# Performance work log

Hardware: AMD Instinct MI355X
Metric: run time of the kernel (lower is better)

The kernel has to match this reference:

```python
import jax, jax.numpy as jnp
import numpy as np

T, B, D, H, L = 512, 128, 256, 256, 4
EPS = 1e-5

def _ln(x, g, b):
    m = jnp.mean(x, axis=-1, keepdims=True)
    v = jnp.mean((x - m) ** 2, axis=-1, keepdims=True)
    return (x - m) * jax.lax.rsqrt(v + EPS) * g + b

def setup_inputs() -> dict:
    key = jax.random.key(0)
    ks = jax.random.split(key, 24)
    s = 0.02
    inp = {
        "x": jax.random.normal(ks[0], (T, B, D), dtype=jnp.float32),
        "lengths": jax.random.randint(ks[1], (B,), 1, T + 1, dtype=jnp.int32),
        # LinearEnchancedGRU params
        "Wr": jax.random.normal(ks[2], (D + H, H)) * s,
        "gr": jnp.ones((H,)), "br": jnp.zeros((H,)),
        "Wz": jax.random.normal(ks[3], (D + H, H)) * s,
        "gz": jnp.ones((H,)), "bz": jnp.zeros((H,)),
        "Wl": jax.random.normal(ks[4], (D + H, H)) * s,
        "gl": jnp.ones((H,)), "bl": jnp.zeros((H,)),
        "Wlt": jax.random.normal(ks[5], (D, H)) * s,
        "Cx": jax.random.normal(ks[6], (D, H)) * s,
        "Ch_w": jax.random.normal(ks[7], (H, H)) * s,
        "Ch_b": jnp.zeros((H,)),
        # TransitionGRU stack params [L, ...]
        "tWr": jax.random.normal(ks[8], (L, H, H)) * s,
        "tgr": jnp.ones((L, H)), "tbr": jnp.zeros((L, H)),
        "tWz": jax.random.normal(ks[9], (L, H, H)) * s,
        "tgz": jnp.ones((L, H)), "tbz": jnp.zeros((L, H)),
        "tWc": jax.random.normal(ks[10], (L, H, H)) * s,
        "tbc": jnp.zeros((L, H)),
    }
    return inp

def reference(x, lengths, Wr, gr, br, Wz, gz, bz, Wl, gl, bl, Wlt, Cx, Ch_w, Ch_b,
              tWr, tgr, tbr, tWz, tgz, tbz, tWc, tbc):
    # x: [T,B,D]; lengths: [B]. Packed-sequence semantics: hidden state of a
    # finished example is frozen; its outputs are zero padding.
    mask = jnp.arange(T, dtype=jnp.int32)[:, None] < lengths[None, :]  # [T,B]

    def cell(xt, h):
        cat = jnp.concatenate([xt, h], axis=-1)  # [B, D+H]
        r = jax.nn.sigmoid(_ln(cat @ Wr, gr, br))
        z = jax.nn.sigmoid(_ln(cat @ Wz, gz, bz))
        l = jax.nn.sigmoid(_ln(cat @ Wl, gl, bl))
        n = jnp.tanh(xt @ Cx + r * (h @ Ch_w + Ch_b)) + l * (xt @ Wlt)
        h = (1.0 - z) * h + z * n
        for i in range(L):  # deep transition stack (fixed small depth)
            ri = jax.nn.sigmoid(_ln(h @ tWr[i], tgr[i], tbr[i]))
            zi = jax.nn.sigmoid(_ln(h @ tWz[i], tgz[i], tbz[i]))
            ni = jnp.tanh(ri * (h @ tWc[i] + tbc[i]))
            h = (1.0 - zi) * ni + zi * h
        return h

    def step(h, inputs):
        xt, mt = inputs  # [B,D], [B]
        hn = cell(xt, h)
        hn = jnp.where(mt[:, None], hn, h)
        out = jnp.where(mt[:, None], hn, 0.0)
        return hn, out

    h0 = jnp.zeros((B, H), dtype=x.dtype)
    _, outs = jax.lax.scan(step, h0, (x, mask))  # outs: [T,B,H]
    return outs
```

## Files before the change

### kernel.cpp

```cpp
#include <hip/hip_runtime.h>
#include <hip/hip_bf16.h>

#define T_ 512
#define B_ 128
#define D_ 256
#define H_ 256
#define EPS 1e-5f

typedef __attribute__((ext_vector_type(8))) short short8;
typedef __attribute__((ext_vector_type(4))) short short4v;
typedef __attribute__((ext_vector_type(4))) float f32x4;

#define SLICE_E  86016
#define WT_TOTAL 1376256

#define STATS_OFFB 2752512UL
#define HX_OFFB    2850816UL
#define FLAG_OFFB  2981888UL
#define NFLAGS     512

#define L_XBF  0
#define L_HBF  8192
#define L_G6   16384
#define L_SRED 22528
#define L_AUX  23040
#define L_TRN  47616
#define L_END  145920

__device__ __forceinline__ short f2bf(float f) {
  unsigned u = __builtin_bit_cast(unsigned, f);
  u = (u + 0x7FFFu + ((u >> 16) & 1u)) >> 16;
  return (short)u;
}
__device__ __forceinline__ f32x4 zero4() { f32x4 z = {0.f, 0.f, 0.f, 0.f}; return z; }
__device__ __forceinline__ f32x4 mfma16(short8 a, short8 b, f32x4 c) {
  return __builtin_amdgcn_mfma_f32_16x16x32_bf16(a, b, c, 0, 0, 0);
}
__device__ __forceinline__ void waitv0() { asm volatile("s_waitcnt vmcnt(0)" ::: "memory"); }

__device__ __forceinline__ f32x4 ald4(float* p) {
  unsigned long long* q = (unsigned long long*)p;
  unsigned long long a = __hip_atomic_load(q,     __ATOMIC_RELAXED, __HIP_MEMORY_SCOPE_AGENT);
  unsigned long long b = __hip_atomic_load(q + 1, __ATOMIC_RELAXED, __HIP_MEMORY_SCOPE_AGENT);
  f32x4 v;
  v[0] = __builtin_bit_cast(float, (unsigned)(a & 0xffffffffu));
  v[1] = __builtin_bit_cast(float, (unsigned)(a >> 32));
  v[2] = __builtin_bit_cast(float, (unsigned)(b & 0xffffffffu));
  v[3] = __builtin_bit_cast(float, (unsigned)(b >> 32));
  return v;
}
__device__ __forceinline__ void ast1f(float* p, float v) {
  __hip_atomic_store((unsigned*)p, __builtin_bit_cast(unsigned, v),
                     __ATOMIC_RELAXED, __HIP_MEMORY_SCOPE_AGENT);
}

__global__ void prep_weights(const float* __restrict__ Wr, const float* __restrict__ Wz,
                             const float* __restrict__ Wl, const float* __restrict__ Wlt,
                             const float* __restrict__ Cx, const float* __restrict__ Chw,
                             const float* __restrict__ tWr, const float* __restrict__ tWz,
                             const float* __restrict__ tWc, short* __restrict__ wt) {
  int idx = blockIdx.x * 256 + threadIdx.x;
  if (idx >= WT_TOTAL) return;
  int j  = idx / SLICE_E;
  int r  = idx - j * SLICE_E;
  int u  = r >> 12;
  int rr = r & 4095;
  int kf = rr >> 9;
  int le = rr & 511;
  int l  = le >> 3, e = le & 7;
  int la = l & 15, lh = l >> 4;
  int col = j * 16 + la;
  float v;
  if (u < 6) {
    int g = u >> 1, half = u & 1;
    int k = half * 256 + lh * 8 + kf * 32 + e;
    const float* W = (g == 0) ? Wr : (g == 1 ? Wz : Wl);
    v = W[k * 256 + col];
  } else if (u < 9) {
    int a = u - 6;
    int k = lh * 8 + kf * 32 + e;
    const float* W = (a == 0) ? Cx : (a == 1 ? Wlt : Chw);
    v = W[k * 256 + col];
  } else {
    int q = u - 9;
    int li = q / 3, m = q - li * 3;
    int k = lh * 8 + kf * 32 + e;
    const float* W = (m == 0) ? tWr : (m == 1 ? tWz : tWc);
    v = W[(li * 256 + k) * 256 + col];
  }
  wt[idx] = f2bf(v);
}

__global__ __launch_bounds__(64)
void rnn_sx(const float* __restrict__ x, const int* __restrict__ lengths,
            const float* __restrict__ gr, const float* __restrict__ br,
            const float* __restrict__ gz, const float* __restrict__ bz,
            const float* __restrict__ gl, const float* __restrict__ bl,
            const float* __restrict__ Chb,
            const float* __restrict__ tgr, const float* __restrict__ tbr,
            const float* __restrict__ tgz, const float* __restrict__ tbz,
            const float* __restrict__ tbc,
            const short* __restrict__ W, float* __restrict__ stats,
            short* __restrict__ hxs, unsigned* __restrict__ flags,
            float* __restrict__ out) {

  __shared__ __align__(16) char smem[L_END];

  const int l  = threadIdx.x;
  const int la = l & 15, lh = l >> 4;
  const int amask = (la & 7) << 4;
  const int bid = blockIdx.x;
  const int cl = bid & 7, j = bid >> 3;
  const int rb0 = cl * 16;
  const int myrow = l >> 2, mc = (l & 3) * 4;
  const int cg = j * 16 + mc;
  const int colb = (l & 3) * 64;

  const short* Wsl = W + (size_t)j * SLICE_E;

  #pragma unroll 1
  for (int u = 0; u < 15; ++u) {
    char* dst = smem + ((u < 3) ? (L_AUX + u * 8192) : (L_TRN + (u - 3) * 8192));
    const short* src = Wsl + (size_t)(u + 6) * 4096;
    #pragma unroll
    for (int kf = 0; kf < 8; ++kf)
      *(short8*)(dst + kf * 1024 + l * 16) = *(const short8*)(src + kf * 512 + l * 8);
  }
  for (int i = l; i < 1024; i += 64) ((short4v*)(smem + L_HBF))[i] = (short4v){0, 0, 0, 0};

  int maxlen = 0;
  for (int i = 0; i < 16; ++i) {
    int v = lengths[rb0 + i];
    maxlen = maxlen > v ? maxlen : v;
  }
  const int mylen = lengths[rb0 + myrow];

  float* stc = stats + (size_t)(cl * 2) * 1536;
  short* hxc = hxs + (size_t)(cl * 2) * 4096;
  unsigned* flc = flags + cl * 64;

  f32x4 hreg = zero4();
  int dead = 0;

  auto pollf = [&](unsigned* fb, unsigned tag) {
    if (!dead) {
      int it = 0;
      while (true) {
        unsigned v = tag;
        if (l < 16) v = __hip_atomic_load(fb + l, __ATOMIC_RELAXED, __HIP_MEMORY_SCOPE_AGENT);
        if (__all((int)(v >= tag))) break;
        if (++it > 300000) { dead = 1; break; }
        __builtin_amdgcn_s_sleep(1);
      }
    }
    asm volatile("" ::: "memory");
  };
  auto ldu = [&](short8 (&dst)[8], const short* bp) {
    #pragma unroll
    for (int kf = 0; kf < 8; ++kf) dst[kf] = *(const short8*)(bp + kf * 512 + l * 8);
  };
  auto mm8r = [&](short8 (&Bv)[8], f32x4& acc, int Ab) {
    #pragma unroll
    for (int kf = 0; kf < 8; ++kf) {
      int aoff = Ab + la * 512 + (((kf * 64) + lh * 16) ^ amask);
      acc = mfma16(*(const short8*)(smem + aoff), Bv[kf], acc);
    }
  };
  auto mmlds = [&](int Bub, f32x4& acc, int Ab) {
    #pragma unroll
    for (int kf = 0; kf < 8; ++kf) {
      int aoff = Ab + la * 512 + (((kf * 64) + lh * 16) ^ amask);
      short8 bv = *(const short8*)(smem + Bub + kf * 1024 + l * 16);
      acc = mfma16(*(const short8*)(smem + aoff), bv, acc);
    }
  };
  auto g6store = [&](int arr, f32x4 acc) {
    #pragma unroll
    for (int i = 0; i < 4; ++i)
      *(float*)(smem + L_G6 + ((arr * 16 + lh * 4 + i) * 16 + la) * 4) = acc[i];
  };
  auto readhx = [&](int par) {
    float* hp = (float*)(hxc + par * 4096 + (l >> 2) * 256 + colb);
    int row2 = l >> 2;
    #pragma unroll
    for (int q2 = 0; q2 < 8; ++q2) {
      f32x4 v = ald4(hp + q2 * 4);
      *(f32x4*)(smem + L_HBF + row2 * 512 + ((colb * 2 + q2 * 16) ^ ((row2 & 7) << 4))) = v;
    }
  };
  auto posth = [&](int par) {
    unsigned long long pk =
        (unsigned long long)(unsigned short)f2bf(hreg[0]) |
        ((unsigned long long)(unsigned short)f2bf(hreg[1]) << 16) |
        ((unsigned long long)(unsigned short)f2bf(hreg[2]) << 32) |
        ((unsigned long long)(unsigned short)f2bf(hreg[3]) << 48);
    __hip_atomic_store((unsigned long long*)(hxc + par * 4096 + myrow * 256 + cg), pk,
                       __ATOMIC_RELAXED, __HIP_MEMORY_SCOPE_AGENT);
  };

  short8 B0[8], B1[8];
  ldu(B0, Wsl);
  ldu(B1, Wsl + 4096);

  for (int t = 0; t < maxlen; ++t) {
    int R = t * 5, par = R & 1;
    {
      const float* xs = x + ((size_t)t * B_ + rb0 + (l >> 2)) * D_ + colb;
      int row2 = l >> 2;
      #pragma unroll
      for (int u2 = 0; u2 < 8; ++u2) {
        f32x4 a = *(const f32x4*)(xs + u2 * 8);
        f32x4 b = *(const f32x4*)(xs + u2 * 8 + 4);
        short8 s;
        s[0] = f2bf(a[0]); s[1] = f2bf(a[1]); s[2] = f2bf(a[2]); s[3] = f2bf(a[3]);
        s[4] = f2bf(b[0]); s[5] = f2bf(b[1]); s[6] = f2bf(b[2]); s[7] = f2bf(b[3]);
        *(short8*)(smem + L_XBF + row2 * 512 + ((colb * 2 + u2 * 16) ^ ((row2 & 7) << 4))) = s;
      }
    }
    f32x4 ac[6];
    #pragma unroll
    for (int a2 = 0; a2 < 6; ++a2) ac[a2] = zero4();
    mm8r(B0, ac[0], L_XBF); ldu(B0, Wsl + 2 * 4096);
    mm8r(B1, ac[0], L_HBF); ldu(B1, Wsl + 3 * 4096);
    mm8r(B0, ac[1], L_XBF); ldu(B0, Wsl + 4 * 4096);
    mm8r(B1, ac[1], L_HBF); ldu(B1, Wsl + 5 * 4096);
    mm8r(B0, ac[2], L_XBF);
    mm8r(B1, ac[2], L_HBF);
    mmlds(L_AUX,         ac[3], L_XBF);
    mmlds(L_AUX + 8192,  ac[4], L_XBF);
    mmlds(L_AUX + 16384, ac[5], L_HBF);
    #pragma unroll
    for (int a2 = 0; a2 < 6; ++a2) g6store(a2, ac[a2]);
    f32x4 pv[6];
    #pragma unroll
    for (int a2 = 0; a2 < 6; ++a2)
      pv[a2] = *(const f32x4*)(smem + L_G6 + ((a2 * 16 + myrow) * 16 + mc) * 4);
    float st[6];
    #pragma unroll
    for (int g2 = 0; g2 < 3; ++g2) {
      f32x4 v = pv[g2];
      st[2 * g2]     = v[0] + v[1] + v[2] + v[3];
      st[2 * g2 + 1] = v[0] * v[0] + v[1] * v[1] + v[2] * v[2] + v[3] * v[3];
    }
    #pragma unroll
    for (int s2 = 0; s2 < 6; ++s2) {
      st[s2] += __shfl_xor(st[s2], 1);
      st[s2] += __shfl_xor(st[s2], 2);
    }
    float* sp = stc + par * 1536;
    {
      int k4 = l & 3;
      ast1f(sp + (k4 * 16 + myrow) * 16 + j, st[k4]);
      if (k4 < 2) ast1f(sp + ((4 + k4) * 16 + myrow) * 16 + j, st[4 + k4]);
    }
    waitv0();
    if (l == 0)
      __hip_atomic_store(flc + par * 16 + j, (unsigned)(R + 1),
                         __ATOMIC_RELAXED, __HIP_MEMORY_SCOPE_AGENT);
    pollf(flc + par * 16, (unsigned)(R + 1));
    {
      float* q = sp + l * 16;
      f32x4 a = ald4(q), b = ald4(q + 4), c = ald4(q + 8), d = ald4(q + 12);
      f32x4 s4 = a + b + c + d;
      *(float*)(smem + L_SRED + l * 4) = s4[0] + s4[1] + s4[2] + s4[3];
      if (l < 32) {
        float* q2 = sp + (64 + l) * 16;
        f32x4 a2 = ald4(q2), b2 = ald4(q2 + 4), c2 = ald4(q2 + 8), d2 = ald4(q2 + 12);
        f32x4 t4 = a2 + b2 + c2 + d2;
        *(float*)(smem + L_SRED + (64 + l) * 4) = t4[0] + t4[1] + t4[2] + t4[3];
      }
    }
    {
      float m3[3], rs3[3];
      #pragma unroll
      for (int g2 = 0; g2 < 3; ++g2) {
        float s1 = *(float*)(smem + L_SRED + ((2 * g2) * 16 + myrow) * 4);
        float s2 = *(float*)(smem + L_SRED + ((2 * g2 + 1) * 16 + myrow) * 4);
        float mm = s1 * (1.f / 256.f);
        float vv = s2 * (1.f / 256.f) - mm * mm;
        m3[g2] = mm; rs3[g2] = rsqrtf((vv > 0.f ? vv : 0.f) + EPS);
      }
      f32x4 g4r = *(const f32x4*)(gr + cg), b4r = *(const f32x4*)(br + cg);
      f32x4 g4z = *(const f32x4*)(gz + cg), b4z = *(const f32x4*)(bz + cg);
      f32x4 g4l = *(const f32x4*)(gl + cg), b4l = *(const f32x4*)(bl + cg);
      f32x4 cb4 = *(const f32x4*)(Chb + cg);
      bool act = t < mylen;
      f32x4 hn;
      #pragma unroll
      for (int q2 = 0; q2 < 4; ++q2) {
        float rv = 1.f / (1.f + __expf(-((pv[0][q2] - m3[0]) * rs3[0] * g4r[q2] + b4r[q2])));
        float zv = 1.f / (1.f + __expf(-((pv[1][q2] - m3[1]) * rs3[1] * g4z[q2] + b4z[q2])));
        float lv = 1.f / (1.f + __expf(-((pv[2][q2] - m3[2]) * rs3[2] * g4l[q2] + b4l[q2])));
        float n = tanhf(pv[3][q2] + rv * (pv[5][q2] + cb4[q2])) + lv * pv[4][q2];
        hn[q2] = (1.f - zv) * hreg[q2] + zv * n;
      }
      if (act) hreg = hn;
    }
    posth(par);
    waitv0();
    if (l == 0)
      __hip_atomic_store(flc + (2 + par) * 16 + j, (unsigned)(R + 1),
                         __ATOMIC_RELAXED, __HIP_MEMORY_SCOPE_AGENT);
    pollf(flc + (2 + par) * 16, (unsigned)(R + 1));
    readhx(par);

    #pragma unroll 1
    for (int li = 0; li < 4; ++li) {
      R = t * 5 + 1 + li; par = R & 1;
      f32x4 tc0 = zero4(), tc1 = zero4(), tc2 = zero4();
      mmlds(L_TRN + (li * 3 + 0) * 8192, tc0, L_HBF);
      mmlds(L_TRN + (li * 3 + 1) * 8192, tc1, L_HBF);
      mmlds(L_TRN + (li * 3 + 2) * 8192, tc2, L_HBF);
      g6store(0, tc0); g6store(1, tc1); g6store(2, tc2);
      f32x4 qv[3];
      #pragma unroll
      for (int a2 = 0; a2 < 3; ++a2)
        qv[a2] = *(const f32x4*)(smem + L_G6 + ((a2 * 16 + myrow) * 16 + mc) * 4);
      float st4[4];
      #pragma unroll
      for (int g2 = 0; g2 < 2; ++g2) {
        f32x4 v = qv[g2];
        st4[2 * g2]     = v[0] + v[1] + v[2] + v[3];
        st4[2 * g2 + 1] = v[0] * v[0] + v[1] * v[1] + v[2] * v[2] + v[3] * v[3];
      }
      #pragma unroll
      for (int s2 = 0; s2 < 4; ++s2) {
        st4[s2] += __shfl_xor(st4[s2], 1);
        st4[s2] += __shfl_xor(st4[s2], 2);
      }
      float* sp2 = stc + par * 1536;
      ast1f(sp2 + ((l & 3) * 16 + myrow) * 16 + j, st4[l & 3]);
      waitv0();
      if (l == 0)
        __hip_atomic_store(flc + par * 16 + j, (unsigned)(R + 1),
                           __ATOMIC_RELAXED, __HIP_MEMORY_SCOPE_AGENT);
      if (li == 3) {
        ldu(B0, Wsl);
        ldu(B1, Wsl + 4096);
      }
      pollf(flc + par * 16, (unsigned)(R + 1));
      {
        float* q = sp2 + l * 16;
        f32x4 a = ald4(q), b = ald4(q + 4), c = ald4(q + 8), d = ald4(q + 12);
        f32x4 s4 = a + b + c + d;
        *(float*)(smem + L_SRED + l * 4) = s4[0] + s4[1] + s4[2] + s4[3];
      }
      bool act = t < mylen;
      {
        float m2[2], rs2[2];
        #pragma unroll
        for (int g2 = 0; g2 < 2; ++g2) {
          float s1 = *(float*)(smem + L_SRED + ((2 * g2) * 16 + myrow) * 4);
          float s2 = *(float*)(smem + L_SRED + ((2 * g2 + 1) * 16 + myrow) * 4);
          float mm = s1 * (1.f / 256.f);
          float vv = s2 * (1.f / 256.f) - mm * mm;
          m2[g2] = mm; rs2[g2] = rsqrtf((vv > 0.f ? vv : 0.f) + EPS);
        }
        f32x4 g4r = *(const f32x4*)(tgr + li * 256 + cg), b4r = *(const f32x4*)(tbr + li * 256 + cg);
        f32x4 g4z = *(const f32x4*)(tgz + li * 256 + cg), b4z = *(const f32x4*)(tbz + li * 256 + cg);
        f32x4 cb4 = *(const f32x4*)(tbc + li * 256 + cg);
        f32x4 hn;
        #pragma unroll
        for (int q2 = 0; q2 < 4; ++q2) {
          float rv = 1.f / (1.f + __expf(-((qv[0][q2] - m2[0]) * rs2[0] * g4r[q2] + b4r[q2])));
          float zv = 1.f / (1.f + __expf(-((qv[1][q2] - m2[1]) * rs2[1] * g4z[q2] + b4z[q2])));
          float n = tanhf(rv * (qv[2][q2] + cb4[q2]));
          hn[q2] = (1.f - zv) * n + zv * hreg[q2];
        }
        if (act) hreg = hn;
        if (li == 3) {
          f32x4 o = act ? hreg : zero4();
          *(f32x4*)(out + ((size_t)t * B_ + rb0 + myrow) * H_ + cg) = o;
        }
      }
      posth(par);
      waitv0();
      if (l == 0)
        __hip_atomic_store(flc + (2 + par) * 16 + j, (unsigned)(R + 1),
                           __ATOMIC_RELAXED, __HIP_MEMORY_SCOPE_AGENT);
      pollf(flc + (2 + par) * 16, (unsigned)(R + 1));
      readhx(par);
    }
  }

  for (int t2 = maxlen; t2 < T_; ++t2)
    *(f32x4*)(out + ((size_t)t2 * B_ + rb0 + myrow) * H_ + cg) = zero4();
}

extern "C" void kernel_launch(void* const* d_in, const int* in_sizes, int n_in,
                              void* d_out, int out_size, void* d_ws, size_t ws_size,
                              hipStream_t stream) {
  const float* x    = (const float*)d_in[0];
  const int* lengths = (const int*)d_in[1];
  const float* Wr   = (const float*)d_in[2];
  const float* gr   = (const float*)d_in[3];
  const float* br   = (const float*)d_in[4];
  const float* Wz   = (const float*)d_in[5];
  const float* gz   = (const float*)d_in[6];
  const float* bz   = (const float*)d_in[7];
  const float* Wl   = (const float*)d_in[8];
  const float* gl   = (const float*)d_in[9];
  const float* bl   = (const float*)d_in[10];
  const float* Wlt  = (const float*)d_in[11];
  const float* Cx   = (const float*)d_in[12];
  const float* Chw  = (const float*)d_in[13];
  const float* Chb  = (const float*)d_in[14];
  const float* tWr  = (const float*)d_in[15];
  const float* tgr  = (const float*)d_in[16];
  const float* tbr  = (const float*)d_in[17];
  const float* tWz  = (const float*)d_in[18];
  const float* tgz  = (const float*)d_in[19];
  const float* tbz  = (const float*)d_in[20];
  const float* tWc  = (const float*)d_in[21];
  const float* tbc  = (const float*)d_in[22];

  short*    wt    = (short*)d_ws;
  float*    stats = (float*)((char*)d_ws + STATS_OFFB);
  short*    hxs   = (short*)((char*)d_ws + HX_OFFB);
  unsigned* flags = (unsigned*)((char*)d_ws + FLAG_OFFB);

  hipMemsetAsync(flags, 0, NFLAGS * sizeof(unsigned), stream);
  hipLaunchKernelGGL(prep_weights, dim3((WT_TOTAL + 255) / 256), dim3(256), 0, stream,
                     Wr, Wz, Wl, Wlt, Cx, Chw, tWr, tWz, tWc, wt);
  hipLaunchKernelGGL(rnn_sx, dim3(128), dim3(64), 0, stream,
                     x, lengths, gr, br, gz, bz, gl, bl, Chb,
                     tgr, tbr, tgz, tbz, tbc, wt, stats, hxs, flags, (float*)d_out);
}
```

Before: 17.77 ms.

## Replace flag-based barriers with tagged data words polled directly

Each 32-bit value exchanged between blocks (LayerNorm partial stats and bf16 hidden-state pairs) is packed into a 64-bit word together with a step tag. Consumers poll the data itself until every tag has reached the current step, so the separate flag store, the vmcnt(0) wait and the flag poll before each read are gone. This takes one global round trip off each of the roughly ten cross-block syncs per timestep. In exchange the exchanged data doubles in size, every poll iteration re-reads and reduces the full data set, and the workspace memset grows.

```diff
diff --git a/kernel.cpp b/kernel.cpp
--- a/kernel.cpp
+++ b/kernel.cpp
@@ -10,14 +10,15 @@
 typedef __attribute__((ext_vector_type(8))) short short8;
 typedef __attribute__((ext_vector_type(4))) short short4v;
 typedef __attribute__((ext_vector_type(4))) float f32x4;
+typedef __attribute__((ext_vector_type(4))) unsigned u32x4;
+typedef unsigned long long ull;
 
 #define SLICE_E  86016
 #define WT_TOTAL 1376256
 
 #define STATS_OFFB 2752512UL
-#define HX_OFFB    2850816UL
-#define FLAG_OFFB  2981888UL
-#define NFLAGS     512
+#define HX_OFFB    2949120UL
+#define SYNC_BYTES 458752UL
 
 #define L_XBF  0
 #define L_HBF  8192
@@ -36,22 +37,14 @@
 __device__ __forceinline__ f32x4 mfma16(short8 a, short8 b, f32x4 c) {
   return __builtin_amdgcn_mfma_f32_16x16x32_bf16(a, b, c, 0, 0, 0);
 }
-__device__ __forceinline__ void waitv0() { asm volatile("s_waitcnt vmcnt(0)" ::: "memory"); }
-
-__device__ __forceinline__ f32x4 ald4(float* p) {
-  unsigned long long* q = (unsigned long long*)p;
-  unsigned long long a = __hip_atomic_load(q,     __ATOMIC_RELAXED, __HIP_MEMORY_SCOPE_AGENT);
-  unsigned long long b = __hip_atomic_load(q + 1, __ATOMIC_RELAXED, __HIP_MEMORY_SCOPE_AGENT);
-  f32x4 v;
-  v[0] = __builtin_bit_cast(float, (unsigned)(a & 0xffffffffu));
-  v[1] = __builtin_bit_cast(float, (unsigned)(a >> 32));
-  v[2] = __builtin_bit_cast(float, (unsigned)(b & 0xffffffffu));
-  v[3] = __builtin_bit_cast(float, (unsigned)(b >> 32));
-  return v;
-}
-__device__ __forceinline__ void ast1f(float* p, float v) {
-  __hip_atomic_store((unsigned*)p, __builtin_bit_cast(unsigned, v),
-                     __ATOMIC_RELAXED, __HIP_MEMORY_SCOPE_AGENT);
+__device__ __forceinline__ ull ald8(ull* p) {
+  return __hip_atomic_load(p, __ATOMIC_RELAXED, __HIP_MEMORY_SCOPE_AGENT);
+}
+__device__ __forceinline__ void ast8(ull* p, ull v) {
+  __hip_atomic_store(p, v, __ATOMIC_RELAXED, __HIP_MEMORY_SCOPE_AGENT);
+}
+__device__ __forceinline__ ull pkf(float v, unsigned tag) {
+  return (ull)__builtin_bit_cast(unsigned, v) | ((ull)tag << 32);
 }
 
 __global__ void prep_weights(const float* __restrict__ Wr, const float* __restrict__ Wz,
@@ -100,9 +93,8 @@
             const float* __restrict__ tgr, const float* __restrict__ tbr,
             const float* __restrict__ tgz, const float* __restrict__ tbz,
             const float* __restrict__ tbc,
-            const short* __restrict__ W, float* __restrict__ stats,
-            short* __restrict__ hxs, unsigned* __restrict__ flags,
-            float* __restrict__ out) {
+            const short* __restrict__ W, ull* __restrict__ st8,
+            ull* __restrict__ hx8, float* __restrict__ out) {
 
   __shared__ __align__(16) char smem[L_END];
 
@@ -135,25 +127,78 @@
   }
   const int mylen = lengths[rb0 + myrow];
 
-  float* stc = stats + (size_t)(cl * 2) * 1536;
-  short* hxc = hxs + (size_t)(cl * 2) * 4096;
-  unsigned* flc = flags + cl * 64;
+  ull* stc = st8 + (size_t)cl * 3072;
+  ull* hxc = hx8 + (size_t)cl * 4096;
 
   f32x4 hreg = zero4();
   int dead = 0;
 
-  auto pollf = [&](unsigned* fb, unsigned tag) {
-    if (!dead) {
-      int it = 0;
-      while (true) {
-        unsigned v = tag;
-        if (l < 16) v = __hip_atomic_load(fb + l, __ATOMIC_RELAXED, __HIP_MEMORY_SCOPE_AGENT);
-        if (__all((int)(v >= tag))) break;
-        if (++it > 300000) { dead = 1; break; }
-        __builtin_amdgcn_s_sleep(1);
-      }
-    }
-    asm volatile("" ::: "memory");
+  auto pollred = [&](int par, unsigned tag, bool g6) {
+    ull* p0 = stc + par * 1536 + l * 16;
+    ull* p1 = stc + par * 1536 + (64 + (l & 31)) * 16;
+    float r0 = 0.f, r1 = 0.f;
+    int it = 0;
+    for (;;) {
+      unsigned mn = 0xffffffffu;
+      float a4[4] = {0.f, 0.f, 0.f, 0.f};
+      #pragma unroll
+      for (int k = 0; k < 16; ++k) {
+        ull v = ald8(p0 + k);
+        a4[k & 3] += __builtin_bit_cast(float, (unsigned)v);
+        unsigned tg = (unsigned)(v >> 32);
+        mn = mn < tg ? mn : tg;
+      }
+      r0 = ((a4[0] + a4[1]) + a4[2]) + a4[3];
+      if (g6 && l < 32) {
+        float b4[4] = {0.f, 0.f, 0.f, 0.f};
+        #pragma unroll
+        for (int k = 0; k < 16; ++k) {
+          ull v = ald8(p1 + k);
+          b4[k & 3] += __builtin_bit_cast(float, (unsigned)v);
+          unsigned tg = (unsigned)(v >> 32);
+          mn = mn < tg ? mn : tg;
+        }
+        r1 = ((b4[0] + b4[1]) + b4[2]) + b4[3];
+      }
+      if (__all((int)(mn >= tag)) || dead) break;
+      if (++it > 200000) dead = 1;
+      __builtin_amdgcn_s_sleep(1);
+    }
+    *(float*)(smem + L_SRED + l * 4) = r0;
+    if (g6 && l < 32) *(float*)(smem + L_SRED + 256 + l * 4) = r1;
+  };
+  auto posth = [&](int par, unsigned tag) {
+    unsigned lo0 = (unsigned)(unsigned short)f2bf(hreg[0]) |
+                   ((unsigned)(unsigned short)f2bf(hreg[1]) << 16);
+    unsigned lo1 = (unsigned)(unsigned short)f2bf(hreg[2]) |
+                   ((unsigned)(unsigned short)f2bf(hreg[3]) << 16);
+    ull* hp = hxc + par * 2048 + myrow * 128 + j * 8 + (l & 3) * 2;
+    ast8(hp,     (ull)lo0 | ((ull)tag << 32));
+    ast8(hp + 1, (ull)lo1 | ((ull)tag << 32));
+  };
+  auto readhx = [&](int par, unsigned tag) {
+    int row2 = l >> 2;
+    ull* hp = hxc + par * 2048 + row2 * 128 + (l & 3) * 32;
+    unsigned lo[32];
+    int it = 0;
+    for (;;) {
+      unsigned mn = 0xffffffffu;
+      #pragma unroll
+      for (int k = 0; k < 32; ++k) {
+        ull v = ald8(hp + k);
+        lo[k] = (unsigned)v;
+        unsigned tg = (unsigned)(v >> 32);
+        mn = mn < tg ? mn : tg;
+      }
+      if (__all((int)(mn >= tag)) || dead) break;
+      if (++it > 200000) dead = 1;
+      __builtin_amdgcn_s_sleep(1);
+    }
+    #pragma unroll
+    for (int q = 0; q < 8; ++q) {
+      u32x4 v = { lo[4 * q], lo[4 * q + 1], lo[4 * q + 2], lo[4 * q + 3] };
+      *(u32x4*)(smem + L_HBF + row2 * 512 + (((l & 3) * 128 + q * 16) ^ ((row2 & 7) << 4))) = v;
+    }
   };
   auto ldu = [&](short8 (&dst)[8], const short* bp) {
     #pragma unroll
@@ -179,24 +224,6 @@
     for (int i = 0; i < 4; ++i)
       *(float*)(smem + L_G6 + ((arr * 16 + lh * 4 + i) * 16 + la) * 4) = acc[i];
   };
-  auto readhx = [&](int par) {
-    float* hp = (float*)(hxc + par * 4096 + (l >> 2) * 256 + colb);
-    int row2 = l >> 2;
-    #pragma unroll
-    for (int q2 = 0; q2 < 8; ++q2) {
-      f32x4 v = ald4(hp + q2 * 4);
-      *(f32x4*)(smem + L_HBF + row2 * 512 + ((colb * 2 + q2 * 16) ^ ((row2 & 7) << 4))) = v;
-    }
-  };
-  auto posth = [&](int par) {
-    unsigned long long pk =
-        (unsigned long long)(unsigned short)f2bf(hreg[0]) |
-        ((unsigned long long)(unsigned short)f2bf(hreg[1]) << 16) |
-        ((unsigned long long)(unsigned short)f2bf(hreg[2]) << 32) |
-        ((unsigned long long)(unsigned short)f2bf(hreg[3]) << 48);
-    __hip_atomic_store((unsigned long long*)(hxc + par * 4096 + myrow * 256 + cg), pk,
-                       __ATOMIC_RELAXED, __HIP_MEMORY_SCOPE_AGENT);
-  };
 
   short8 B0[8], B1[8];
   ldu(B0, Wsl);
@@ -204,6 +231,7 @@
 
   for (int t = 0; t < maxlen; ++t) {
     int R = t * 5, par = R & 1;
+    unsigned tag = (unsigned)(R + 1);
     {
       const float* xs = x + ((size_t)t * B_ + rb0 + (l >> 2)) * D_ + colb;
       int row2 = l >> 2;
@@ -247,29 +275,13 @@
       st[s2] += __shfl_xor(st[s2], 1);
       st[s2] += __shfl_xor(st[s2], 2);
     }
-    float* sp = stc + par * 1536;
     {
+      ull* sp = stc + par * 1536;
       int k4 = l & 3;
-      ast1f(sp + (k4 * 16 + myrow) * 16 + j, st[k4]);
-      if (k4 < 2) ast1f(sp + ((4 + k4) * 16 + myrow) * 16 + j, st[4 + k4]);
-    }
-    waitv0();
-    if (l == 0)
-      __hip_atomic_store(flc + par * 16 + j, (unsigned)(R + 1),
-                         __ATOMIC_RELAXED, __HIP_MEMORY_SCOPE_AGENT);
-    pollf(flc + par * 16, (unsigned)(R + 1));
-    {
-      float* q = sp + l * 16;
-      f32x4 a = ald4(q), b = ald4(q + 4), c = ald4(q + 8), d = ald4(q + 12);
-      f32x4 s4 = a + b + c + d;
-      *(float*)(smem + L_SRED + l * 4) = s4[0] + s4[1] + s4[2] + s4[3];
-      if (l < 32) {
-        float* q2 = sp + (64 + l) * 16;
-        f32x4 a2 = ald4(q2), b2 = ald4(q2 + 4), c2 = ald4(q2 + 8), d2 = ald4(q2 + 12);
-        f32x4 t4 = a2 + b2 + c2 + d2;
-        *(float*)(smem + L_SRED + (64 + l) * 4) = t4[0] + t4[1] + t4[2] + t4[3];
-      }
-    }
+      ast8(sp + (k4 * 16 + myrow) * 16 + j, pkf(st[k4], tag));
+      if (k4 < 2) ast8(sp + ((4 + k4) * 16 + myrow) * 16 + j, pkf(st[4 + k4], tag));
+    }
+    pollred(par, tag, true);
     {
       float m3[3], rs3[3];
       #pragma unroll
@@ -296,17 +308,12 @@
       }
       if (act) hreg = hn;
     }
-    posth(par);
-    waitv0();
-    if (l == 0)
-      __hip_atomic_store(flc + (2 + par) * 16 + j, (unsigned)(R + 1),
-                         __ATOMIC_RELAXED, __HIP_MEMORY_SCOPE_AGENT);
-    pollf(flc + (2 + par) * 16, (unsigned)(R + 1));
-    readhx(par);
+    posth(par, tag);
+    readhx(par, tag);
 
     #pragma unroll 1
     for (int li = 0; li < 4; ++li) {
-      R = t * 5 + 1 + li; par = R & 1;
+      R = t * 5 + 1 + li; par = R & 1; tag = (unsigned)(R + 1);
       f32x4 tc0 = zero4(), tc1 = zero4(), tc2 = zero4();
       mmlds(L_TRN + (li * 3 + 0) * 8192, tc0, L_HBF);
       mmlds(L_TRN + (li * 3 + 1) * 8192, tc1, L_HBF);
@@ -328,23 +335,12 @@
         st4[s2] += __shfl_xor(st4[s2], 1);
         st4[s2] += __shfl_xor(st4[s2], 2);
       }
-      float* sp2 = stc + par * 1536;
-      ast1f(sp2 + ((l & 3) * 16 + myrow) * 16 + j, st4[l & 3]);
-      waitv0();
-      if (l == 0)
-        __hip_atomic_store(flc + par * 16 + j, (unsigned)(R + 1),
-                           __ATOMIC_RELAXED, __HIP_MEMORY_SCOPE_AGENT);
+      ast8(stc + par * 1536 + ((l & 3) * 16 + myrow) * 16 + j, pkf(st4[l & 3], tag));
       if (li == 3) {
         ldu(B0, Wsl);
         ldu(B1, Wsl + 4096);
       }
-      pollf(flc + par * 16, (unsigned)(R + 1));
-      {
-        float* q = sp2 + l * 16;
-        f32x4 a = ald4(q), b = ald4(q + 4), c = ald4(q + 8), d = ald4(q + 12);
-        f32x4 s4 = a + b + c + d;
-        *(float*)(smem + L_SRED + l * 4) = s4[0] + s4[1] + s4[2] + s4[3];
-      }
+      pollred(par, tag, false);
       bool act = t < mylen;
       {
         float m2[2], rs2[2];
@@ -373,13 +369,8 @@
           *(f32x4*)(out + ((size_t)t * B_ + rb0 + myrow) * H_ + cg) = o;
         }
       }
-      posth(par);
-      waitv0();
-      if (l == 0)
-        __hip_atomic_store(flc + (2 + par) * 16 + j, (unsigned)(R + 1),
-                           __ATOMIC_RELAXED, __HIP_MEMORY_SCOPE_AGENT);
-      pollf(flc + (2 + par) * 16, (unsigned)(R + 1));
-      readhx(par);
+      posth(par, tag);
+      readhx(par, tag);
     }
   }
 
@@ -414,15 +405,14 @@
   const float* tWc  = (const float*)d_in[21];
   const float* tbc  = (const float*)d_in[22];
 
-  short*    wt    = (short*)d_ws;
-  float*    stats = (float*)((char*)d_ws + STATS_OFFB);
-  short*    hxs   = (short*)((char*)d_ws + HX_OFFB);
-  unsigned* flags = (unsigned*)((char*)d_ws + FLAG_OFFB);
-
-  hipMemsetAsync(flags, 0, NFLAGS * sizeof(unsigned), stream);
+  short* wt  = (short*)d_ws;
+  ull*   st8 = (ull*)((char*)d_ws + STATS_OFFB);
+  ull*   hx8 = (ull*)((char*)d_ws + HX_OFFB);
+
+  hipMemsetAsync((char*)d_ws + STATS_OFFB, 0, SYNC_BYTES, stream);
   hipLaunchKernelGGL(prep_weights, dim3((WT_TOTAL + 255) / 256), dim3(256), 0, stream,
                      Wr, Wz, Wl, Wlt, Cx, Chw, tWr, tWz, tWc, wt);
   hipLaunchKernelGGL(rnn_sx, dim3(128), dim3(64), 0, stream,
                      x, lengths, gr, br, gz, bz, gl, bl, Chb,
-                     tgr, tbr, tgz, tbz, tbc, wt, stats, hxs, flags, (float*)d_out);
-}
+                     tgr, tbr, tgz, tbz, tbc, wt, st8, hx8, (float*)d_out);
+}
```

Measured after the change: 26.88 ms. +51.2%, slower.

## Interleave two batch clusters per block to overlap cross-block sync with compute

Applied to the files above, without the earlier changes.

Each workgroup now handles two 16-row batch clusters (A and B) for its column slice, so 64 blocks run instead of 128. The A and B work is interleaved: while waiting on cluster A's cross-block flags, the block computes B's matmuls, which hides the spin-wait latency. Flags move to per-block padded slots (stride 16 words), so each lane polls its own cache line instead of a whole wave polling with __all. In exchange, per-block serial work doubles and LDS use grows to hold two hidden-state buffers.

```diff
diff --git a/kernel.cpp b/kernel.cpp
--- a/kernel.cpp
+++ b/kernel.cpp
@@ -10,6 +10,7 @@
 typedef __attribute__((ext_vector_type(8))) short short8;
 typedef __attribute__((ext_vector_type(4))) short short4v;
 typedef __attribute__((ext_vector_type(4))) float f32x4;
+typedef unsigned long long ull;
 
 #define SLICE_E  86016
 #define WT_TOTAL 1376256
@@ -17,15 +18,16 @@
 #define STATS_OFFB 2752512UL
 #define HX_OFFB    2850816UL
 #define FLAG_OFFB  2981888UL
-#define NFLAGS     512
+#define FLAG_BYTES 32768UL
 
 #define L_XBF  0
-#define L_HBF  8192
-#define L_G6   16384
-#define L_SRED 22528
-#define L_AUX  23040
-#define L_TRN  47616
-#define L_END  145920
+#define L_HBFA 8192
+#define L_HBFB 16384
+#define L_G6   24576
+#define L_SRED 30720
+#define L_AUX  31232
+#define L_TRN  55808
+#define L_END  154112
 
 __device__ __forceinline__ short f2bf(float f) {
   unsigned u = __builtin_bit_cast(unsigned, f);
@@ -39,9 +41,9 @@
 __device__ __forceinline__ void waitv0() { asm volatile("s_waitcnt vmcnt(0)" ::: "memory"); }
 
 __device__ __forceinline__ f32x4 ald4(float* p) {
-  unsigned long long* q = (unsigned long long*)p;
-  unsigned long long a = __hip_atomic_load(q,     __ATOMIC_RELAXED, __HIP_MEMORY_SCOPE_AGENT);
-  unsigned long long b = __hip_atomic_load(q + 1, __ATOMIC_RELAXED, __HIP_MEMORY_SCOPE_AGENT);
+  ull* q = (ull*)p;
+  ull a = __hip_atomic_load(q,     __ATOMIC_RELAXED, __HIP_MEMORY_SCOPE_AGENT);
+  ull b = __hip_atomic_load(q + 1, __ATOMIC_RELAXED, __HIP_MEMORY_SCOPE_AGENT);
   f32x4 v;
   v[0] = __builtin_bit_cast(float, (unsigned)(a & 0xffffffffu));
   v[1] = __builtin_bit_cast(float, (unsigned)(a >> 32));
@@ -52,6 +54,9 @@
 __device__ __forceinline__ void ast1f(float* p, float v) {
   __hip_atomic_store((unsigned*)p, __builtin_bit_cast(unsigned, v),
                      __ATOMIC_RELAXED, __HIP_MEMORY_SCOPE_AGENT);
+}
+__device__ __forceinline__ void ast8(ull* p, ull v) {
+  __hip_atomic_store(p, v, __ATOMIC_RELAXED, __HIP_MEMORY_SCOPE_AGENT);
 }
 
 __global__ void prep_weights(const float* __restrict__ Wr, const float* __restrict__ Wz,
@@ -92,7 +97,7 @@
 }
 
 __global__ __launch_bounds__(64)
-void rnn_sx(const float* __restrict__ x, const int* __restrict__ lengths,
+void rnn_mx(const float* __restrict__ x, const int* __restrict__ lengths,
             const float* __restrict__ gr, const float* __restrict__ br,
             const float* __restrict__ gz, const float* __restrict__ bz,
             const float* __restrict__ gl, const float* __restrict__ bl,
@@ -110,8 +115,9 @@
   const int la = l & 15, lh = l >> 4;
   const int amask = (la & 7) << 4;
   const int bid = blockIdx.x;
-  const int cl = bid & 7, j = bid >> 3;
-  const int rb0 = cl * 16;
+  const int clA = bid & 3, clB = 4 + clA;
+  const int j   = bid >> 2;
+  const int rb0A = clA * 16, rb0B = clB * 16;
   const int myrow = l >> 2, mc = (l & 3) * 4;
   const int cg = j * 16 + mc;
   const int colb = (l & 3) * 64;
@@ -126,34 +132,71 @@
     for (int kf = 0; kf < 8; ++kf)
       *(short8*)(dst + kf * 1024 + l * 16) = *(const short8*)(src + kf * 512 + l * 8);
   }
-  for (int i = l; i < 1024; i += 64) ((short4v*)(smem + L_HBF))[i] = (short4v){0, 0, 0, 0};
+  for (int i = l; i < 1024; i += 64) {
+    ((short4v*)(smem + L_HBFA))[i] = (short4v){0, 0, 0, 0};
+    ((short4v*)(smem + L_HBFB))[i] = (short4v){0, 0, 0, 0};
+  }
 
   int maxlen = 0;
   for (int i = 0; i < 16; ++i) {
-    int v = lengths[rb0 + i];
-    maxlen = maxlen > v ? maxlen : v;
-  }
-  const int mylen = lengths[rb0 + myrow];
-
-  float* stc = stats + (size_t)(cl * 2) * 1536;
-  short* hxc = hxs + (size_t)(cl * 2) * 4096;
-  unsigned* flc = flags + cl * 64;
-
-  f32x4 hreg = zero4();
+    int va = lengths[rb0A + i], vb = lengths[rb0B + i];
+    int m = va > vb ? va : vb;
+    maxlen = maxlen > m ? maxlen : m;
+  }
+  const int mylenA = lengths[rb0A + myrow];
+  const int mylenB = lengths[rb0B + myrow];
+
+  float* stcA = stats + (size_t)(clA * 2) * 1536;
+  float* stcB = stats + (size_t)(clB * 2) * 1536;
+  short* hxcA = hxs + (size_t)(clA * 2) * 4096;
+  short* hxcB = hxs + (size_t)(clB * 2) * 4096;
+  unsigned* flcA = flags + clA * 1024;
+  unsigned* flcB = flags + clB * 1024;
+
   int dead = 0;
 
-  auto pollf = [&](unsigned* fb, unsigned tag) {
-    if (!dead) {
+  auto postflag = [&](unsigned* flc, int fam, int par, unsigned tag) {
+    if (l == 0)
+      __hip_atomic_store(flc + (fam * 2 + par) * 256 + j * 16, tag,
+                         __ATOMIC_RELAXED, __HIP_MEMORY_SCOPE_AGENT);
+  };
+  auto pollf = [&](unsigned* flc, int fam, int par, unsigned tag) {
+    if (!dead && l < 16) {
+      unsigned* sp = flc + (fam * 2 + par) * 256 + l * 16;
       int it = 0;
-      while (true) {
-        unsigned v = tag;
-        if (l < 16) v = __hip_atomic_load(fb + l, __ATOMIC_RELAXED, __HIP_MEMORY_SCOPE_AGENT);
-        if (__all((int)(v >= tag))) break;
+      while (__hip_atomic_load(sp, __ATOMIC_RELAXED, __HIP_MEMORY_SCOPE_AGENT) < tag) {
         if (++it > 300000) { dead = 1; break; }
         __builtin_amdgcn_s_sleep(1);
       }
     }
     asm volatile("" ::: "memory");
+  };
+  auto redstats = [&](float* sp, bool both) {
+    float* q = sp + l * 16;
+    f32x4 a = ald4(q), b = ald4(q + 4), c = ald4(q + 8), d = ald4(q + 12);
+    f32x4 s4 = a + b + c + d;
+    *(float*)(smem + L_SRED + l * 4) = s4[0] + s4[1] + s4[2] + s4[3];
+    if (both && l < 32) {
+      float* q2 = sp + (64 + l) * 16;
+      f32x4 a2 = ald4(q2), b2 = ald4(q2 + 4), c2 = ald4(q2 + 8), d2 = ald4(q2 + 12);
+      f32x4 t4 = a2 + b2 + c2 + d2;
+      *(float*)(smem + L_SRED + (64 + l) * 4) = t4[0] + t4[1] + t4[2] + t4[3];
+    }
+  };
+  auto posth = [&](short* hxc, int par, f32x4 h) {
+    ull pk = (ull)(unsigned short)f2bf(h[0]) |
+             ((ull)(unsigned short)f2bf(h[1]) << 16) |
+             ((ull)(unsigned short)f2bf(h[2]) << 32) |
+             ((ull)(unsigned short)f2bf(h[3]) << 48);
+    ast8((ull*)(hxc + par * 4096 + myrow * 256 + cg), pk);
+  };
+  auto readhx = [&](short* hxc, int par, int hbfB) {
+    float* hp = (float*)(hxc + par * 4096 + myrow * 256 + colb);
+    #pragma unroll
+    for (int q2 = 0; q2 < 8; ++q2) {
+      f32x4 v = ald4(hp + q2 * 4);
+      *(f32x4*)(smem + hbfB + myrow * 512 + ((colb * 2 + q2 * 16) ^ ((myrow & 7) << 4))) = v;
+    }
   };
   auto ldu = [&](short8 (&dst)[8], const short* bp) {
     #pragma unroll
@@ -179,62 +222,52 @@
     for (int i = 0; i < 4; ++i)
       *(float*)(smem + L_G6 + ((arr * 16 + lh * 4 + i) * 16 + la) * 4) = acc[i];
   };
-  auto readhx = [&](int par) {
-    float* hp = (float*)(hxc + par * 4096 + (l >> 2) * 256 + colb);
-    int row2 = l >> 2;
-    #pragma unroll
-    for (int q2 = 0; q2 < 8; ++q2) {
-      f32x4 v = ald4(hp + q2 * 4);
-      *(f32x4*)(smem + L_HBF + row2 * 512 + ((colb * 2 + q2 * 16) ^ ((row2 & 7) << 4))) = v;
-    }
-  };
-  auto posth = [&](int par) {
-    unsigned long long pk =
-        (unsigned long long)(unsigned short)f2bf(hreg[0]) |
-        ((unsigned long long)(unsigned short)f2bf(hreg[1]) << 16) |
-        ((unsigned long long)(unsigned short)f2bf(hreg[2]) << 32) |
-        ((unsigned long long)(unsigned short)f2bf(hreg[3]) << 48);
-    __hip_atomic_store((unsigned long long*)(hxc + par * 4096 + myrow * 256 + cg), pk,
-                       __ATOMIC_RELAXED, __HIP_MEMORY_SCOPE_AGENT);
-  };
 
   short8 B0[8], B1[8];
   ldu(B0, Wsl);
   ldu(B1, Wsl + 4096);
 
-  for (int t = 0; t < maxlen; ++t) {
-    int R = t * 5, par = R & 1;
-    {
-      const float* xs = x + ((size_t)t * B_ + rb0 + (l >> 2)) * D_ + colb;
-      int row2 = l >> 2;
-      #pragma unroll
-      for (int u2 = 0; u2 < 8; ++u2) {
-        f32x4 a = *(const f32x4*)(xs + u2 * 8);
-        f32x4 b = *(const f32x4*)(xs + u2 * 8 + 4);
-        short8 s;
-        s[0] = f2bf(a[0]); s[1] = f2bf(a[1]); s[2] = f2bf(a[2]); s[3] = f2bf(a[3]);
-        s[4] = f2bf(b[0]); s[5] = f2bf(b[1]); s[6] = f2bf(b[2]); s[7] = f2bf(b[3]);
-        *(short8*)(smem + L_XBF + row2 * 512 + ((colb * 2 + u2 * 16) ^ ((row2 & 7) << 4))) = s;
-      }
-    }
+  auto stageX = [&](int t, int rb0c) {
+    const float* xs = x + ((size_t)t * B_ + rb0c + myrow) * D_ + colb;
+    #pragma unroll
+    for (int u2 = 0; u2 < 8; ++u2) {
+      f32x4 a = *(const f32x4*)(xs + u2 * 8);
+      f32x4 b = *(const f32x4*)(xs + u2 * 8 + 4);
+      short8 s;
+      s[0] = f2bf(a[0]); s[1] = f2bf(a[1]); s[2] = f2bf(a[2]); s[3] = f2bf(a[3]);
+      s[4] = f2bf(b[0]); s[5] = f2bf(b[1]); s[6] = f2bf(b[2]); s[7] = f2bf(b[3]);
+      *(short8*)(smem + L_XBF + myrow * 512 + ((colb * 2 + u2 * 16) ^ ((myrow & 7) << 4))) = s;
+    }
+  };
+  auto gmm = [&](int hbfB, bool trailing) {
     f32x4 ac[6];
     #pragma unroll
     for (int a2 = 0; a2 < 6; ++a2) ac[a2] = zero4();
     mm8r(B0, ac[0], L_XBF); ldu(B0, Wsl + 2 * 4096);
-    mm8r(B1, ac[0], L_HBF); ldu(B1, Wsl + 3 * 4096);
+    mm8r(B1, ac[0], hbfB);  ldu(B1, Wsl + 3 * 4096);
     mm8r(B0, ac[1], L_XBF); ldu(B0, Wsl + 4 * 4096);
-    mm8r(B1, ac[1], L_HBF); ldu(B1, Wsl + 5 * 4096);
+    mm8r(B1, ac[1], hbfB);  ldu(B1, Wsl + 5 * 4096);
     mm8r(B0, ac[2], L_XBF);
-    mm8r(B1, ac[2], L_HBF);
+    mm8r(B1, ac[2], hbfB);
     mmlds(L_AUX,         ac[3], L_XBF);
     mmlds(L_AUX + 8192,  ac[4], L_XBF);
-    mmlds(L_AUX + 16384, ac[5], L_HBF);
+    mmlds(L_AUX + 16384, ac[5], hbfB);
+    if (trailing) { ldu(B0, Wsl); ldu(B1, Wsl + 4096); }
     #pragma unroll
     for (int a2 = 0; a2 < 6; ++a2) g6store(a2, ac[a2]);
-    f32x4 pv[6];
-    #pragma unroll
-    for (int a2 = 0; a2 < 6; ++a2)
+  };
+  auto tmm = [&](int li, int hbfB) {
+    f32x4 t0 = zero4(), t1 = zero4(), t2 = zero4();
+    mmlds(L_TRN + (li * 3 + 0) * 8192, t0, hbfB);
+    mmlds(L_TRN + (li * 3 + 1) * 8192, t1, hbfB);
+    mmlds(L_TRN + (li * 3 + 2) * 8192, t2, hbfB);
+    g6store(0, t0); g6store(1, t1); g6store(2, t2);
+  };
+  auto pvread = [&](f32x4* pv, int n) {
+    for (int a2 = 0; a2 < n; ++a2)
       pv[a2] = *(const f32x4*)(smem + L_G6 + ((a2 * 16 + myrow) * 16 + mc) * 4);
+  };
+  auto statG = [&](float* sp, f32x4 (&pv)[6]) {
     float st[6];
     #pragma unroll
     for (int g2 = 0; g2 < 3; ++g2) {
@@ -247,144 +280,154 @@
       st[s2] += __shfl_xor(st[s2], 1);
       st[s2] += __shfl_xor(st[s2], 2);
     }
-    float* sp = stc + par * 1536;
-    {
-      int k4 = l & 3;
-      ast1f(sp + (k4 * 16 + myrow) * 16 + j, st[k4]);
-      if (k4 < 2) ast1f(sp + ((4 + k4) * 16 + myrow) * 16 + j, st[4 + k4]);
-    }
+    int k4 = l & 3;
+    ast1f(sp + (k4 * 16 + myrow) * 16 + j, st[k4]);
+    if (k4 < 2) ast1f(sp + ((4 + k4) * 16 + myrow) * 16 + j, st[4 + k4]);
+  };
+  auto statT = [&](float* sp, f32x4 (&qv)[3]) {
+    float st4[4];
+    #pragma unroll
+    for (int g2 = 0; g2 < 2; ++g2) {
+      f32x4 v = qv[g2];
+      st4[2 * g2]     = v[0] + v[1] + v[2] + v[3];
+      st4[2 * g2 + 1] = v[0] * v[0] + v[1] * v[1] + v[2] * v[2] + v[3] * v[3];
+    }
+    #pragma unroll
+    for (int s2 = 0; s2 < 4; ++s2) {
+      st4[s2] += __shfl_xor(st4[s2], 1);
+      st4[s2] += __shfl_xor(st4[s2], 2);
+    }
+    ast1f(sp + ((l & 3) * 16 + myrow) * 16 + j, st4[l & 3]);
+  };
+  auto elemG = [&](f32x4 (&pv)[6], f32x4& hreg, int mylen, int t) {
+    float m3[3], rs3[3];
+    #pragma unroll
+    for (int g2 = 0; g2 < 3; ++g2) {
+      float s1 = *(float*)(smem + L_SRED + ((2 * g2) * 16 + myrow) * 4);
+      float s2 = *(float*)(smem + L_SRED + ((2 * g2 + 1) * 16 + myrow) * 4);
+      float mm = s1 * (1.f / 256.f);
+      float vv = s2 * (1.f / 256.f) - mm * mm;
+      m3[g2] = mm; rs3[g2] = rsqrtf((vv > 0.f ? vv : 0.f) + EPS);
+    }
+    f32x4 g4r = *(const f32x4*)(gr + cg), b4r = *(const f32x4*)(br + cg);
+    f32x4 g4z = *(const f32x4*)(gz + cg), b4z = *(const f32x4*)(bz + cg);
+    f32x4 g4l = *(const f32x4*)(gl + cg), b4l = *(const f32x4*)(bl + cg);
+    f32x4 cb4 = *(const f32x4*)(Chb + cg);
+    f32x4 hn;
+    #pragma unroll
+    for (int q2 = 0; q2 < 4; ++q2) {
+      float rv = 1.f / (1.f + __expf(-((pv[0][q2] - m3[0]) * rs3[0] * g4r[q2] + b4r[q2])));
+      float zv = 1.f / (1.f + __expf(-((pv[1][q2] - m3[1]) * rs3[1] * g4z[q2] + b4z[q2])));
+      float lv = 1.f / (1.f + __expf(-((pv[2][q2] - m3[2]) * rs3[2] * g4l[q2] + b4l[q2])));
+      float n = tanhf(pv[3][q2] + rv * (pv[5][q2] + cb4[q2])) + lv * pv[4][q2];
+      hn[q2] = (1.f - zv) * hreg[q2] + zv * n;
+    }
+    if (t < mylen) hreg = hn;
+  };
+  auto elemT = [&](f32x4 (&qv)[3], f32x4& hreg, int li, int mylen, int t, int rb0c) {
+    float m2[2], rs2[2];
+    #pragma unroll
+    for (int g2 = 0; g2 < 2; ++g2) {
+      float s1 = *(float*)(smem + L_SRED + ((2 * g2) * 16 + myrow) * 4);
+      float s2 = *(float*)(smem + L_SRED + ((2 * g2 + 1) * 16 + myrow) * 4);
+      float mm = s1 * (1.f / 256.f);
+      float vv = s2 * (1.f / 256.f) - mm * mm;
+      m2[g2] = mm; rs2[g2] = rsqrtf((vv > 0.f ? vv : 0.f) + EPS);
+    }
+    f32x4 g4r = *(const f32x4*)(tgr + li * 256 + cg), b4r = *(const f32x4*)(tbr + li * 256 + cg);
+    f32x4 g4z = *(const f32x4*)(tgz + li * 256 + cg), b4z = *(const f32x4*)(tbz + li * 256 + cg);
+    f32x4 cb4 = *(const f32x4*)(tbc + li * 256 + cg);
+    bool act = t < mylen;
+    f32x4 hn;
+    #pragma unroll
+    for (int q2 = 0; q2 < 4; ++q2) {
+      float rv = 1.f / (1.f + __expf(-((qv[0][q2] - m2[0]) * rs2[0] * g4r[q2] + b4r[q2])));
+      float zv = 1.f / (1.f + __expf(-((qv[1][q2] - m2[1]) * rs2[1] * g4z[q2] + b4z[q2])));
+      float n = tanhf(rv * (qv[2][q2] + cb4[q2]));
+      hn[q2] = (1.f - zv) * n + zv * hreg[q2];
+    }
+    if (act) hreg = hn;
+    if (li == 3) {
+      f32x4 o = act ? hreg : zero4();
+      *(f32x4*)(out + ((size_t)t * B_ + rb0c + myrow) * H_ + cg) = o;
+    }
+  };
+
+  f32x4 hregA = zero4(), hregB = zero4();
+
+  for (int t = 0; t < maxlen; ++t) {
+    int R = t * 5, par = R & 1;
+    unsigned tag = (unsigned)(R + 1);
+    f32x4 pvA[6], pvB[6];
+
+    stageX(t, rb0A);
+    gmm(L_HBFA, true);
+    pvread(pvA, 6);
+    statG(stcA + par * 1536, pvA);
+    stageX(t, rb0B);
+    gmm(L_HBFB, false);
     waitv0();
-    if (l == 0)
-      __hip_atomic_store(flc + par * 16 + j, (unsigned)(R + 1),
-                         __ATOMIC_RELAXED, __HIP_MEMORY_SCOPE_AGENT);
-    pollf(flc + par * 16, (unsigned)(R + 1));
-    {
-      float* q = sp + l * 16;
-      f32x4 a = ald4(q), b = ald4(q + 4), c = ald4(q + 8), d = ald4(q + 12);
-      f32x4 s4 = a + b + c + d;
-      *(float*)(smem + L_SRED + l * 4) = s4[0] + s4[1] + s4[2] + s4[3];
-      if (l < 32) {
-        float* q2 = sp + (64 + l) * 16;
-        f32x4 a2 = ald4(q2), b2 = ald4(q2 + 4), c2 = ald4(q2 + 8), d2 = ald4(q2 + 12);
-        f32x4 t4 = a2 + b2 + c2 + d2;
-        *(float*)(smem + L_SRED + (64 + l) * 4) = t4[0] + t4[1] + t4[2] + t4[3];
-      }
-    }
-    {
-      float m3[3], rs3[3];
-      #pragma unroll
-      for (int g2 = 0; g2 < 3; ++g2) {
-        float s1 = *(float*)(smem + L_SRED + ((2 * g2) * 16 + myrow) * 4);
-        float s2 = *(float*)(smem + L_SRED + ((2 * g2 + 1) * 16 + myrow) * 4);
-        float mm = s1 * (1.f / 256.f);
-        float vv = s2 * (1.f / 256.f) - mm * mm;
-        m3[g2] = mm; rs3[g2] = rsqrtf((vv > 0.f ? vv : 0.f) + EPS);
-      }
-      f32x4 g4r = *(const f32x4*)(gr + cg), b4r = *(const f32x4*)(br + cg);
-      f32x4 g4z = *(const f32x4*)(gz + cg), b4z = *(const f32x4*)(bz + cg);
-      f32x4 g4l = *(const f32x4*)(gl + cg), b4l = *(const f32x4*)(bl + cg);
-      f32x4 cb4 = *(const f32x4*)(Chb + cg);
-      bool act = t < mylen;
-      f32x4 hn;
-      #pragma unroll
-      for (int q2 = 0; q2 < 4; ++q2) {
-        float rv = 1.f / (1.f + __expf(-((pv[0][q2] - m3[0]) * rs3[0] * g4r[q2] + b4r[q2])));
-        float zv = 1.f / (1.f + __expf(-((pv[1][q2] - m3[1]) * rs3[1] * g4z[q2] + b4z[q2])));
-        float lv = 1.f / (1.f + __expf(-((pv[2][q2] - m3[2]) * rs3[2] * g4l[q2] + b4l[q2])));
-        float n = tanhf(pv[3][q2] + rv * (pv[5][q2] + cb4[q2])) + lv * pv[4][q2];
-        hn[q2] = (1.f - zv) * hreg[q2] + zv * n;
-      }
-      if (act) hreg = hn;
-    }
-    posth(par);
+    postflag(flcA, 0, par, tag);
+    pvread(pvB, 6);
+    statG(stcB + par * 1536, pvB);
     waitv0();
-    if (l == 0)
-      __hip_atomic_store(flc + (2 + par) * 16 + j, (unsigned)(R + 1),
-                         __ATOMIC_RELAXED, __HIP_MEMORY_SCOPE_AGENT);
-    pollf(flc + (2 + par) * 16, (unsigned)(R + 1));
-    readhx(par);
+    postflag(flcB, 0, par, tag);
+
+    pollf(flcA, 0, par, tag);
+    redstats(stcA + par * 1536, true);
+    elemG(pvA, hregA, mylenA, t);
+    posth(hxcA, par, hregA);
+    pollf(flcB, 0, par, tag);
+    redstats(stcB + par * 1536, true);
+    elemG(pvB, hregB, mylenB, t);
+    posth(hxcB, par, hregB);
+    waitv0();
+    postflag(flcA, 1, par, tag);
+    postflag(flcB, 1, par, tag);
+    pollf(flcA, 1, par, tag);
+    readhx(hxcA, par, L_HBFA);
+    pollf(flcB, 1, par, tag);
+    readhx(hxcB, par, L_HBFB);
 
     #pragma unroll 1
     for (int li = 0; li < 4; ++li) {
-      R = t * 5 + 1 + li; par = R & 1;
-      f32x4 tc0 = zero4(), tc1 = zero4(), tc2 = zero4();
-      mmlds(L_TRN + (li * 3 + 0) * 8192, tc0, L_HBF);
-      mmlds(L_TRN + (li * 3 + 1) * 8192, tc1, L_HBF);
-      mmlds(L_TRN + (li * 3 + 2) * 8192, tc2, L_HBF);
-      g6store(0, tc0); g6store(1, tc1); g6store(2, tc2);
-      f32x4 qv[3];
-      #pragma unroll
-      for (int a2 = 0; a2 < 3; ++a2)
-        qv[a2] = *(const f32x4*)(smem + L_G6 + ((a2 * 16 + myrow) * 16 + mc) * 4);
-      float st4[4];
-      #pragma unroll
-      for (int g2 = 0; g2 < 2; ++g2) {
-        f32x4 v = qv[g2];
-        st4[2 * g2]     = v[0] + v[1] + v[2] + v[3];
-        st4[2 * g2 + 1] = v[0] * v[0] + v[1] * v[1] + v[2] * v[2] + v[3] * v[3];
-      }
-      #pragma unroll
-      for (int s2 = 0; s2 < 4; ++s2) {
-        st4[s2] += __shfl_xor(st4[s2], 1);
-        st4[s2] += __shfl_xor(st4[s2], 2);
-      }
-      float* sp2 = stc + par * 1536;
-      ast1f(sp2 + ((l & 3) * 16 + myrow) * 16 + j, st4[l & 3]);
+      R = t * 5 + 1 + li; par = R & 1; tag = (unsigned)(R + 1);
+      f32x4 qvA[3], qvB[3];
+
+      tmm(li, L_HBFA);
+      pvread(qvA, 3);
+      statT(stcA + par * 1536, qvA);
+      tmm(li, L_HBFB);
       waitv0();
-      if (l == 0)
-        __hip_atomic_store(flc + par * 16 + j, (unsigned)(R + 1),
-                           __ATOMIC_RELAXED, __HIP_MEMORY_SCOPE_AGENT);
-      if (li == 3) {
-        ldu(B0, Wsl);
-        ldu(B1, Wsl + 4096);
-      }
-      pollf(flc + par * 16, (unsigned)(R + 1));
-      {
-        float* q = sp2 + l * 16;
-        f32x4 a = ald4(q), b = ald4(q + 4), c = ald4(q + 8), d = ald4(q + 12);
-        f32x4 s4 = a + b + c + d;
-        *(float*)(smem + L_SRED + l * 4) = s4[0] + s4[1] + s4[2] + s4[3];
-      }
-      bool act = t < mylen;
-      {
-        float m2[2], rs2[2];
-        #pragma unroll
-        for (int g2 = 0; g2 < 2; ++g2) {
-          float s1 = *(float*)(smem + L_SRED + ((2 * g2) * 16 + myrow) * 4);
-          float s2 = *(float*)(smem + L_SRED + ((2 * g2 + 1) * 16 + myrow) * 4);
-          float mm = s1 * (1.f / 256.f);
-          float vv = s2 * (1.f / 256.f) - mm * mm;
-          m2[g2] = mm; rs2[g2] = rsqrtf((vv > 0.f ? vv : 0.f) + EPS);
-        }
-        f32x4 g4r = *(const f32x4*)(tgr + li * 256 + cg), b4r = *(const f32x4*)(tbr + li * 256 + cg);
-        f32x4 g4z = *(const f32x4*)(tgz + li * 256 + cg), b4z = *(const f32x4*)(tbz + li * 256 + cg);
-        f32x4 cb4 = *(const f32x4*)(tbc + li * 256 + cg);
-        f32x4 hn;
-        #pragma unroll
-        for (int q2 = 0; q2 < 4; ++q2) {
-          float rv = 1.f / (1.f + __expf(-((qv[0][q2] - m2[0]) * rs2[0] * g4r[q2] + b4r[q2])));
-          float zv = 1.f / (1.f + __expf(-((qv[1][q2] - m2[1]) * rs2[1] * g4z[q2] + b4z[q2])));
-          float n = tanhf(rv * (qv[2][q2] + cb4[q2]));
-          hn[q2] = (1.f - zv) * n + zv * hreg[q2];
-        }
-        if (act) hreg = hn;
-        if (li == 3) {
-          f32x4 o = act ? hreg : zero4();
-          *(f32x4*)(out + ((size_t)t * B_ + rb0 + myrow) * H_ + cg) = o;
-        }
-      }
-      posth(par);
+      postflag(flcA, 0, par, tag);
+      pvread(qvB, 3);
+      statT(stcB + par * 1536, qvB);
       waitv0();
-      if (l == 0)
-        __hip_atomic_store(flc + (2 + par) * 16 + j, (unsigned)(R + 1),
-                           __ATOMIC_RELAXED, __HIP_MEMORY_SCOPE_AGENT);
-      pollf(flc + (2 + par) * 16, (unsigned)(R + 1));
-      readhx(par);
-    }
-  }
-
-  for (int t2 = maxlen; t2 < T_; ++t2)
-    *(f32x4*)(out + ((size_t)t2 * B_ + rb0 + myrow) * H_ + cg) = zero4();
+      postflag(flcB, 0, par, tag);
+
+      pollf(flcA, 0, par, tag);
+      redstats(stcA + par * 1536, false);
+      elemT(qvA, hregA, li, mylenA, t, rb0A);
+      posth(hxcA, par, hregA);
+      pollf(flcB, 0, par, tag);
+      redstats(stcB + par * 1536, false);
+      elemT(qvB, hregB, li, mylenB, t, rb0B);
+      posth(hxcB, par, hregB);
+      waitv0();
+      postflag(flcA, 1, par, tag);
+      postflag(flcB, 1, par, tag);
+      if (li == 3) { ldu(B0, Wsl); ldu(B1, Wsl + 4096); }
+      pollf(flcA, 1, par, tag);
+      readhx(hxcA, par, L_HBFA);
+      pollf(flcB, 1, par, tag);
+      readhx(hxcB, par, L_HBFB);
+    }
+  }
+
+  for (int t2 = maxlen; t2 < T_; ++t2) {
+    *(f32x4*)(out + ((size_t)t2 * B_ + rb0A + myrow) * H_ + cg) = zero4();
+    *(f32x4*)(out + ((size_t)t2 * B_ + rb0B + myrow) * H_ + cg) = zero4();
+  }
 }
 
 extern "C" void kernel_launch(void* const* d_in, const int* in_sizes, int n_in,
@@ -419,10 +462,10 @@
   short*    hxs   = (short*)((char*)d_ws + HX_OFFB);
   unsigned* flags = (unsigned*)((char*)d_ws + FLAG_OFFB);
 
-  hipMemsetAsync(flags, 0, NFLAGS * sizeof(unsigned), stream);
+  hipMemsetAsync(flags, 0, FLAG_BYTES, stream);
   hipLaunchKernelGGL(prep_weights, dim3((WT_TOTAL + 255) / 256), dim3(256), 0, stream,
                      Wr, Wz, Wl, Wlt, Cx, Chw, tWr, tWz, tWc, wt);
-  hipLaunchKernelGGL(rnn_sx, dim3(128), dim3(64), 0, stream,
+  hipLaunchKernelGGL(rnn_mx, dim3(64), dim3(64), 0, stream,
                      x, lengths, gr, br, gz, bz, gl, bl, Chb,
                      tgr, tbr, tgz, tbz, tbc, wt, stats, hxs, flags, (float*)d_out);
 }
```

After: 25.44 ms. 43.1% more time.
